# Kernel tuning notes

Hardware: AMD Instinct MI355X
Metric: run time of the kernel (lower is better)

Reference implementation:

```python
import jax, jax.numpy as jnp
import numpy as np

D_MODEL = 768
D_STATE = 16
B, L = 4, 2048


def setup_inputs() -> dict:
    key = jax.random.key(0)
    ks = jax.random.split(key, 8)
    s = 1.0 / np.sqrt(D_MODEL)
    x = jax.random.normal(ks[0], (B, L, D_MODEL), jnp.float32)
    W_in = jax.random.normal(ks[1], (D_MODEL, 2 * D_MODEL), jnp.float32) * s
    b_in = jnp.zeros((2 * D_MODEL,), jnp.float32)
    W_B = jax.random.normal(ks[2], (D_MODEL, D_STATE), jnp.float32) * s
    b_B = jnp.zeros((D_STATE,), jnp.float32)
    W_C = jax.random.normal(ks[3], (D_MODEL, D_STATE), jnp.float32) * s
    b_C = jnp.zeros((D_STATE,), jnp.float32)
    W_delta = jax.random.normal(ks[4], (D_MODEL, D_MODEL), jnp.float32) * s
    b_delta = jnp.zeros((D_MODEL,), jnp.float32)
    W_out = jax.random.normal(ks[5], (D_MODEL, D_MODEL), jnp.float32) * s
    b_out = jnp.zeros((D_MODEL,), jnp.float32)
    # A_log init from the module: log(A + 1) with A[s, d] = s+1
    A_log = jnp.log(jnp.arange(1, D_STATE + 1, dtype=jnp.float32)[:, None]
                    * jnp.ones((1, D_MODEL), jnp.float32) + 1.0)
    D = jnp.ones((D_MODEL,), jnp.float32)
    return {"x": x, "W_in": W_in, "b_in": b_in, "W_B": W_B, "b_B": b_B,
            "W_C": W_C, "b_C": b_C, "W_delta": W_delta, "b_delta": b_delta,
            "W_out": W_out, "b_out": b_out, "A_log": A_log, "D": D}


def reference(x, W_in, b_in, W_B, b_B, W_C, b_C, W_delta, b_delta,
              W_out, b_out, A_log, D):
    x_proj = x @ W_in + b_in                      # (B, L, 2*d_model)
    x_main, x_gate = jnp.split(x_proj, 2, axis=-1)
    x_main = jax.nn.silu(x_main)
    B_mat = x_main @ W_B + b_B                    # (B, L, d_state)
    C_mat = x_main @ W_C + b_C                    # (B, L, d_state)
    delta = jax.nn.softplus(x_main @ W_delta + b_delta) + 0.0001
    delta = jnp.clip(delta, 0.0001, 1.0)          # (B, L, d_model)
    A = jnp.clip(-jnp.exp(A_log), -5.0, -0.1)     # (d_state, d_model)
    deltaA = jnp.exp(jnp.clip(delta[:, :, None, :] * A[None, None, :, :], -2.0, 0.0))
    deltaA = jnp.clip(deltaA, 0.05, 1.0)          # (B, L, d_state, d_model)
    deltaB_u = jnp.clip(delta[:, :, None, :] * B_mat[:, :, :, None] * x_main[:, :, None, :],
                        -5.0, 5.0)                # (B, L, d_state, d_model)

    def binary_operator(elem1, elem2):
        A1, Bu1 = elem1
        A2, Bu2 = elem2
        A_c = jnp.clip(A2 * A1, 1e-06, 10.0)
        Bu_c = jnp.clip(A2 * Bu1 + Bu2, -100.0, 100.0)
        return (A_c, Bu_c)

    # elementwise combine => scanning along axis=1 of the batched arrays is
    # identical to vmapping a per-batch scan over axis 0
    _, h_Bu = jax.lax.associative_scan(binary_operator, (deltaA, deltaB_u), axis=1)
    y = jnp.einsum('blsd,bls->bld', h_Bu, C_mat)
    y = jnp.clip(y, -10.0, 10.0)
    y = y + x_main * D[None, None, :]
    y = y * jax.nn.silu(x_gate)
    y = jnp.clip(y @ W_out + b_out, -10.0, 10.0)
    return y
```

## Files before the change

kernel.cpp:

```cpp
#include <hip/hip_runtime.h>
#include <hip/hip_bf16.h>
#include <cstdint>
#include <cstddef>

#define D_MODEL 768
#define D_STATE 16
#define BB      4
#define LL      2048
#define M_TOT   (BB*LL)
#define NCHUNK  64
#define LCH     (LL/NCHUNK)
#define N_DBC   896

typedef __attribute__((ext_vector_type(8))) short bf16x8;
typedef __attribute__((ext_vector_type(4))) float f32x4;

__device__ __forceinline__ float clampf_(float x, float lo, float hi) {
    return fminf(fmaxf(x, lo), hi);
}
__device__ __forceinline__ float siluf_(float x) {
    return x / (1.f + __expf(-x));
}
__device__ __forceinline__ unsigned short f2bf(float f) {
    unsigned u = __float_as_uint(f);
    u += 0x7fffu + ((u >> 16) & 1u);
    return (unsigned short)(u >> 16);
}
__device__ __forceinline__ float bf2f(unsigned short u) {
    return __uint_as_float(((unsigned)u) << 16);
}
__device__ __forceinline__ void gload16(void* lds, const void* g) {
    __builtin_amdgcn_global_load_lds(
        (const __attribute__((address_space(1))) void*)g,
        (__attribute__((address_space(3))) void*)lds, 16, 0, 0);
}


__global__ __launch_bounds__(256) void k_convert_x(const float* __restrict__ x,
                                                   unsigned short* __restrict__ xb, int n4) {
    int i = blockIdx.x * 256 + threadIdx.x;
    if (i >= n4) return;
    float4 v = ((const float4*)x)[i];
    ushort4 o;
    o.x = f2bf(v.x); o.y = f2bf(v.y); o.z = f2bf(v.z); o.w = f2bf(v.w);
    ((ushort4*)xb)[i] = o;
}

__global__ __launch_bounds__(256) void k_prep_A(const float* __restrict__ A_log,
                                                float* __restrict__ A_cl, int n) {
    int i = blockIdx.x * 256 + threadIdx.x;
    if (i < n) A_cl[i] = clampf_(-__expf(A_log[i]), -5.f, -0.1f);
}

__global__ __launch_bounds__(256) void k_transpose_bf16(const float* __restrict__ src,
                                                        unsigned short* __restrict__ dst,
                                                        int R, int C) {
    __shared__ float tile[32][33];
    int tx = threadIdx.x & 31, ty = threadIdx.x >> 5;
    int c0 = blockIdx.x * 32, r0 = blockIdx.y * 32;
    #pragma unroll
    for (int rr = ty; rr < 32; rr += 8)
        tile[rr][tx] = src[(size_t)(r0 + rr) * C + c0 + tx];
    __syncthreads();
    #pragma unroll
    for (int rr = ty; rr < 32; rr += 8)
        dst[(size_t)(c0 + rr) * R + r0 + tx] = f2bf(tile[tx][rr]);
}

__global__ __launch_bounds__(256) void k_fill_bc(const float* __restrict__ W_B,
                                                 const float* __restrict__ W_C,
                                                 unsigned short* __restrict__ WdBC) {
    int idx = blockIdx.x * 256 + threadIdx.x;
    if (idx >= 128 * D_MODEL) return;
    int r = idx / D_MODEL + D_MODEL, k = idx % D_MODEL;
    unsigned short v = 0;
    if (r < D_MODEL + 16)       v = f2bf(W_B[k * 16 + (r - D_MODEL)]);
    else if (r < D_MODEL + 32)  v = f2bf(W_C[k * 16 + (r - D_MODEL - 16)]);
    WdBC[(size_t)r * D_MODEL + k] = v;
}

__global__ __launch_bounds__(256) void k_bias_dbc(const float* __restrict__ b_delta,
                                                  const float* __restrict__ b_B,
                                                  const float* __restrict__ b_C,
                                                  float* __restrict__ bias) {
    int i = blockIdx.x * 256 + threadIdx.x;
    if (i >= N_DBC) return;
    float v = 0.f;
    if (i < D_MODEL)            v = b_delta[i];
    else if (i < D_MODEL + 16)  v = b_B[i - D_MODEL];
    else if (i < D_MODEL + 32)  v = b_C[i - D_MODEL - 16];
    bias[i] = v;
}

template<int EPI>
__global__ __launch_bounds__(256) void k_gemm(const unsigned short* __restrict__ A,
                                              const unsigned short* __restrict__ Bt,
                                              const float* __restrict__ bias,
                                              int K,
                                              float* __restrict__ out_f,
                                              float* __restrict__ out_f2,
                                              unsigned short* __restrict__ out_b0,
                                              unsigned short* __restrict__ out_b1) {
    __shared__ __align__(16) unsigned short As[128 * 32];
    __shared__ __align__(16) unsigned short Bs[128 * 32];
    const int tid = threadIdx.x;
    const int wave = tid >> 6, lane = tid & 63;
    const int wm = wave >> 1, wn = wave & 1;
    const int m0 = blockIdx.y * 128, n0 = blockIdx.x * 128;
    const int lr = lane & 15, lk = (lane >> 4) * 8;

    f32x4 acc[4][4] = {};

    for (int kt = 0; kt < K; kt += 32) {
        #pragma unroll
        for (int p = 0; p < 2; ++p) {
            int ci = p * 256 + wave * 64 + lane;
            int row = ci >> 2, k8 = (ci & 3) * 8;
            const unsigned short* ga = &A [(size_t)(m0 + row) * K + kt + k8];
            const unsigned short* gb = &Bt[(size_t)(n0 + row) * K + kt + k8];
            gload16(&As[(p * 256 + wave * 64) * 8], ga);
            gload16(&Bs[(p * 256 + wave * 64) * 8], gb);
        }
        __syncthreads();

        bf16x8 af[4], bfr[4];
        #pragma unroll
        for (int mt = 0; mt < 4; ++mt)
            af[mt] = *(const bf16x8*)&As[(wm * 64 + mt * 16 + lr) * 32 + lk];
        #pragma unroll
        for (int nt = 0; nt < 4; ++nt)
            bfr[nt] = *(const bf16x8*)&Bs[(wn * 64 + nt * 16 + lr) * 32 + lk];
        #pragma unroll
        for (int mt = 0; mt < 4; ++mt)
            #pragma unroll
            for (int nt = 0; nt < 4; ++nt)
                acc[mt][nt] = __builtin_amdgcn_mfma_f32_16x16x32_bf16(
                    af[mt], bfr[nt], acc[mt][nt], 0, 0, 0);
        __syncthreads();
    }

    #pragma unroll
    for (int mt = 0; mt < 4; ++mt) {
        int row = m0 + wm * 64 + mt * 16 + (lane >> 4) * 4;
        #pragma unroll
        for (int nt = 0; nt < 4; ++nt) {
            int col = n0 + wn * 64 + nt * 16 + (lane & 15);
            #pragma unroll
            for (int i = 0; i < 4; ++i) {
                int r = row + i;
                float v = acc[mt][nt][i] + bias[col];
                if (EPI == 0) {
                    float s = siluf_(v);
                    if (col < D_MODEL) out_b0[(size_t)r * D_MODEL + col] = f2bf(s);
                    else               out_b1[(size_t)r * D_MODEL + (col - D_MODEL)] = f2bf(s);
                } else if (EPI == 1) {
                    if (col < D_MODEL) {
                        float sp = (v > 20.f) ? v : log1pf(__expf(v));
                        out_b0[(size_t)r * D_MODEL + col] = f2bf(clampf_(sp + 1e-4f, 1e-4f, 1.f));
                    } else if (col < D_MODEL + 16) {
                        out_f[(size_t)r * D_STATE + (col - D_MODEL)] = v;
                    } else if (col < D_MODEL + 32) {
                        out_f2[(size_t)r * D_STATE + (col - D_MODEL - 16)] = v;
                    }
                } else {
                    out_f[(size_t)r * D_MODEL + col] = clampf_(v, -10.f, 10.f);
                }
            }
        }
    }
}

__global__ __launch_bounds__(256) void k_scanA(const unsigned short* __restrict__ dlt,
                                               const unsigned short* __restrict__ xm,
                                               const float* __restrict__ Bm,
                                               const float* __restrict__ A_cl,
                                               float* __restrict__ h_end,
                                               float* __restrict__ Aprod) {
    const int d = blockIdx.x * 256 + threadIdx.x;
    const int c = blockIdx.y, b = blockIdx.z;
    __shared__ float Bsh[LCH][D_STATE];
    const int rowbase = b * LL + c * LCH;
    for (int i = threadIdx.x; i < LCH * D_STATE; i += 256)
        ((float*)Bsh)[i] = Bm[(size_t)rowbase * D_STATE + i];
    __syncthreads();

    float Asv[16], h[16], ap[16];
    #pragma unroll
    for (int s = 0; s < 16; ++s) {
        Asv[s] = A_cl[s * D_MODEL + d];
        h[s] = 0.f; ap[s] = 1.f;
    }
    for (int tt = 0; tt < LCH; ++tt) {
        const size_t rowoff = (size_t)(rowbase + tt);
        float dltv = bf2f(dlt[rowoff * D_MODEL + d]);
        float xv   = bf2f(xm [rowoff * D_MODEL + d]);
        float dx = dltv * xv;
        #pragma unroll
        for (int s = 0; s < 16; ++s) {
            float dA  = __expf(fmaxf(dltv * Asv[s], -2.f));
            float dBu = clampf_(dx * Bsh[tt][s], -5.f, 5.f);
            h[s] = clampf_(fmaf(dA, h[s], dBu), -100.f, 100.f);
            ap[s] *= dA;
        }
    }
    const size_t off = (((size_t)b * NCHUNK + c) * D_STATE) * D_MODEL + d;
    #pragma unroll
    for (int s = 0; s < 16; ++s) {
        h_end[off + (size_t)s * D_MODEL] = h[s];
        Aprod[off + (size_t)s * D_MODEL] = ap[s];
    }
}

__global__ __launch_bounds__(256) void k_scanB(const float* __restrict__ h_end,
                                               const float* __restrict__ Aprod,
                                               float* __restrict__ h_in) {
    const int idx = blockIdx.x * 256 + threadIdx.x;
    const int d = idx % D_MODEL;
    const int rest = idx / D_MODEL;
    const int s = rest & 15, b = rest >> 4;
    float hc = 0.f;
    for (int c = 0; c < NCHUNK; ++c) {
        const size_t off = (((size_t)b * NCHUNK + c) * D_STATE + s) * D_MODEL + d;
        h_in[off] = hc;
        hc = Aprod[off] * hc + h_end[off];
    }
}

__global__ __launch_bounds__(256) void k_scanC(const unsigned short* __restrict__ dlt,
                                               const unsigned short* __restrict__ xm,
                                               const float* __restrict__ Bm,
                                               const float* __restrict__ Cm,
                                               const float* __restrict__ A_cl,
                                               const float* __restrict__ h_in,
                                               const float* __restrict__ Dvec,
                                               const unsigned short* __restrict__ gate,
                                               unsigned short* __restrict__ ymid) {
    const int d = blockIdx.x * 256 + threadIdx.x;
    const int c = blockIdx.y, b = blockIdx.z;
    __shared__ float Bsh[LCH][D_STATE];
    __shared__ float Csh[LCH][D_STATE];
    const int rowbase = b * LL + c * LCH;
    for (int i = threadIdx.x; i < LCH * D_STATE; i += 256) {
        ((float*)Bsh)[i] = Bm[(size_t)rowbase * D_STATE + i];
        ((float*)Csh)[i] = Cm[(size_t)rowbase * D_STATE + i];
    }
    __syncthreads();

    float Asv[16], h[16];
    const size_t coff = (((size_t)b * NCHUNK + c) * D_STATE) * D_MODEL + d;
    #pragma unroll
    for (int s = 0; s < 16; ++s) {
        Asv[s] = A_cl[s * D_MODEL + d];
        h[s] = h_in[coff + (size_t)s * D_MODEL];
    }
    const float Dv = Dvec[d];
    for (int tt = 0; tt < LCH; ++tt) {
        const size_t rowoff = (size_t)(rowbase + tt);
        float dltv = bf2f(dlt[rowoff * D_MODEL + d]);
        float xv   = bf2f(xm [rowoff * D_MODEL + d]);
        float dx = dltv * xv;
        float y = 0.f;
        #pragma unroll
        for (int s = 0; s < 16; ++s) {
            float dA  = __expf(fmaxf(dltv * Asv[s], -2.f));
            float dBu = clampf_(dx * Bsh[tt][s], -5.f, 5.f);
            h[s] = clampf_(fmaf(dA, h[s], dBu), -100.f, 100.f);
            y = fmaf(h[s], Csh[tt][s], y);
        }
        y = clampf_(y, -10.f, 10.f);
        y = fmaf(xv, Dv, y);
        y *= bf2f(gate[rowoff * D_MODEL + d]);
        ymid[rowoff * D_MODEL + d] = f2bf(y);
    }
}

extern "C" void kernel_launch(void* const* d_in, const int* in_sizes, int n_in,
                              void* d_out, int out_size, void* d_ws, size_t ws_size,
                              hipStream_t stream) {
    const float* x       = (const float*)d_in[0];
    const float* W_in    = (const float*)d_in[1];
    const float* b_in    = (const float*)d_in[2];
    const float* W_B     = (const float*)d_in[3];
    const float* b_B     = (const float*)d_in[4];
    const float* W_C     = (const float*)d_in[5];
    const float* b_C     = (const float*)d_in[6];
    const float* W_delta = (const float*)d_in[7];
    const float* b_delta = (const float*)d_in[8];
    const float* W_out   = (const float*)d_in[9];
    const float* b_out   = (const float*)d_in[10];
    const float* A_log   = (const float*)d_in[11];
    const float* Dvec    = (const float*)d_in[12];
    float* out = (float*)d_out;

    char* p = (char*)d_ws;
    auto alloc = [&](size_t bytes) {
        char* r = p;
        p += (bytes + 255) & ~(size_t)255;
        return r;
    };
    unsigned short* xb    = (unsigned short*)alloc((size_t)M_TOT * D_MODEL * 2);
    unsigned short* Wint  = (unsigned short*)alloc((size_t)2 * D_MODEL * D_MODEL * 2);
    unsigned short* WdBC  = (unsigned short*)alloc((size_t)N_DBC * D_MODEL * 2);
    unsigned short* Wot   = (unsigned short*)alloc((size_t)D_MODEL * D_MODEL * 2);
    float*          bdbc  = (float*)alloc((size_t)N_DBC * 4);
    unsigned short* xm_b  = (unsigned short*)alloc((size_t)M_TOT * D_MODEL * 2);
    unsigned short* gate_b= (unsigned short*)alloc((size_t)M_TOT * D_MODEL * 2);
    unsigned short* dlt_b = (unsigned short*)alloc((size_t)M_TOT * D_MODEL * 2);
    float*          Bm    = (float*)alloc((size_t)M_TOT * D_STATE * 4);
    float*          Cm    = (float*)alloc((size_t)M_TOT * D_STATE * 4);
    float*          A_cl  = (float*)alloc((size_t)D_STATE * D_MODEL * 4);
    float*          h_end = (float*)alloc((size_t)BB * NCHUNK * D_STATE * D_MODEL * 4);
    float*          Aprod = (float*)alloc((size_t)BB * NCHUNK * D_STATE * D_MODEL * 4);
    float*          h_in  = (float*)alloc((size_t)BB * NCHUNK * D_STATE * D_MODEL * 4);
    unsigned short* ymid  = (unsigned short*)alloc((size_t)M_TOT * D_MODEL * 2);

    k_convert_x<<<(M_TOT * D_MODEL / 4 + 255) / 256, 256, 0, stream>>>(x, xb, M_TOT * D_MODEL / 4);
    k_prep_A<<<(D_STATE * D_MODEL + 255) / 256, 256, 0, stream>>>(A_log, A_cl, D_STATE * D_MODEL);
    k_transpose_bf16<<<dim3(2 * D_MODEL / 32, D_MODEL / 32), 256, 0, stream>>>(W_in, Wint, D_MODEL, 2 * D_MODEL);
    k_transpose_bf16<<<dim3(D_MODEL / 32, D_MODEL / 32), 256, 0, stream>>>(W_delta, WdBC, D_MODEL, D_MODEL);
    k_fill_bc<<<(128 * D_MODEL + 255) / 256, 256, 0, stream>>>(W_B, W_C, WdBC);
    k_bias_dbc<<<(N_DBC + 255) / 256, 256, 0, stream>>>(b_delta, b_B, b_C, bdbc);
    k_transpose_bf16<<<dim3(D_MODEL / 32, D_MODEL / 32), 256, 0, stream>>>(W_out, Wot, D_MODEL, D_MODEL);

    k_gemm<0><<<dim3(2 * D_MODEL / 128, M_TOT / 128), 256, 0, stream>>>(
        xb, Wint, b_in, D_MODEL, nullptr, nullptr, xm_b, gate_b);
    k_gemm<1><<<dim3(N_DBC / 128, M_TOT / 128), 256, 0, stream>>>(
        xm_b, WdBC, bdbc, D_MODEL, Bm, Cm, dlt_b, nullptr);
    k_scanA<<<dim3(D_MODEL / 256, NCHUNK, BB), 256, 0, stream>>>(dlt_b, xm_b, Bm, A_cl, h_end, Aprod);
    k_scanB<<<(BB * D_STATE * D_MODEL) / 256, 256, 0, stream>>>(h_end, Aprod, h_in);
    k_scanC<<<dim3(D_MODEL / 256, NCHUNK, BB), 256, 0, stream>>>(
        dlt_b, xm_b, Bm, Cm, A_cl, h_in, Dvec, gate_b, ymid);
    k_gemm<2><<<dim3(D_MODEL / 128, M_TOT / 128), 256, 0, stream>>>(
        ymid, Wot, b_out, D_MODEL, out, nullptr, nullptr, nullptr);
}
```

Baseline: 224.1 us.

## Double-buffer GEMM LDS tiles and swizzle workgroup order across XCDs

```diff
diff --git a/kernel.cpp b/kernel.cpp
--- a/kernel.cpp
+++ b/kernel.cpp
@@ -96,48 +96,67 @@
 __global__ __launch_bounds__(256) void k_gemm(const unsigned short* __restrict__ A,
                                               const unsigned short* __restrict__ Bt,
                                               const float* __restrict__ bias,
-                                              int K,
+                                              int K, int gx,
                                               float* __restrict__ out_f,
                                               float* __restrict__ out_f2,
                                               unsigned short* __restrict__ out_b0,
                                               unsigned short* __restrict__ out_b1) {
-    __shared__ __align__(16) unsigned short As[128 * 32];
-    __shared__ __align__(16) unsigned short Bs[128 * 32];
+    __shared__ __align__(16) unsigned short As[2][128 * 32];
+    __shared__ __align__(16) unsigned short Bs[2][128 * 32];
     const int tid = threadIdx.x;
     const int wave = tid >> 6, lane = tid & 63;
     const int wm = wave >> 1, wn = wave & 1;
-    const int m0 = blockIdx.y * 128, n0 = blockIdx.x * 128;
+
+    const int nwg = gridDim.x;
+    const int wg = blockIdx.x;
+    int swz = wg;
+    if ((nwg & 7) == 0) {
+        const int q = nwg >> 3;
+        swz = (wg & 7) * q + (wg >> 3);
+    }
+    const int bx = swz % gx, by = swz / gx;
+    const int m0 = by * 128, n0 = bx * 128;
     const int lr = lane & 15, lk = (lane >> 4) * 8;
 
     f32x4 acc[4][4] = {};
 
-    for (int kt = 0; kt < K; kt += 32) {
+    auto stage = [&](int buf, int kt) {
         #pragma unroll
         for (int p = 0; p < 2; ++p) {
             int ci = p * 256 + wave * 64 + lane;
             int row = ci >> 2, k8 = (ci & 3) * 8;
-            const unsigned short* ga = &A [(size_t)(m0 + row) * K + kt + k8];
-            const unsigned short* gb = &Bt[(size_t)(n0 + row) * K + kt + k8];
-            gload16(&As[(p * 256 + wave * 64) * 8], ga);
-            gload16(&Bs[(p * 256 + wave * 64) * 8], gb);
+            gload16(&As[buf][(p * 256 + wave * 64) * 8],
+                    &A [(size_t)(m0 + row) * K + kt + k8]);
+            gload16(&Bs[buf][(p * 256 + wave * 64) * 8],
+                    &Bt[(size_t)(n0 + row) * K + kt + k8]);
         }
-        __syncthreads();
-
+    };
+    auto compute = [&](int buf) {
         bf16x8 af[4], bfr[4];
         #pragma unroll
         for (int mt = 0; mt < 4; ++mt)
-            af[mt] = *(const bf16x8*)&As[(wm * 64 + mt * 16 + lr) * 32 + lk];
+            af[mt] = *(const bf16x8*)&As[buf][(wm * 64 + mt * 16 + lr) * 32 + lk];
         #pragma unroll
         for (int nt = 0; nt < 4; ++nt)
-            bfr[nt] = *(const bf16x8*)&Bs[(wn * 64 + nt * 16 + lr) * 32 + lk];
+            bfr[nt] = *(const bf16x8*)&Bs[buf][(wn * 64 + nt * 16 + lr) * 32 + lk];
         #pragma unroll
         for (int mt = 0; mt < 4; ++mt)
             #pragma unroll
             for (int nt = 0; nt < 4; ++nt)
                 acc[mt][nt] = __builtin_amdgcn_mfma_f32_16x16x32_bf16(
                     af[mt], bfr[nt], acc[mt][nt], 0, 0, 0);
+    };
+
+    stage(0, 0);
+    __syncthreads();
+    int cur = 0;
+    for (int kt = 32; kt < K; kt += 32) {
+        stage(cur ^ 1, kt);
+        compute(cur);
         __syncthreads();
-    }
+        cur ^= 1;
+    }
+    compute(cur);
 
     #pragma unroll
     for (int mt = 0; mt < 4; ++mt) {
@@ -322,14 +341,14 @@
     k_bias_dbc<<<(N_DBC + 255) / 256, 256, 0, stream>>>(b_delta, b_B, b_C, bdbc);
     k_transpose_bf16<<<dim3(D_MODEL / 32, D_MODEL / 32), 256, 0, stream>>>(W_out, Wot, D_MODEL, D_MODEL);
 
-    k_gemm<0><<<dim3(2 * D_MODEL / 128, M_TOT / 128), 256, 0, stream>>>(
-        xb, Wint, b_in, D_MODEL, nullptr, nullptr, xm_b, gate_b);
-    k_gemm<1><<<dim3(N_DBC / 128, M_TOT / 128), 256, 0, stream>>>(
-        xm_b, WdBC, bdbc, D_MODEL, Bm, Cm, dlt_b, nullptr);
+    k_gemm<0><<<dim3((2 * D_MODEL / 128) * (M_TOT / 128)), 256, 0, stream>>>(
+        xb, Wint, b_in, D_MODEL, 2 * D_MODEL / 128, nullptr, nullptr, xm_b, gate_b);
+    k_gemm<1><<<dim3((N_DBC / 128) * (M_TOT / 128)), 256, 0, stream>>>(
+        xm_b, WdBC, bdbc, D_MODEL, N_DBC / 128, Bm, Cm, dlt_b, nullptr);
     k_scanA<<<dim3(D_MODEL / 256, NCHUNK, BB), 256, 0, stream>>>(dlt_b, xm_b, Bm, A_cl, h_end, Aprod);
     k_scanB<<<(BB * D_STATE * D_MODEL) / 256, 256, 0, stream>>>(h_end, Aprod, h_in);
     k_scanC<<<dim3(D_MODEL / 256, NCHUNK, BB), 256, 0, stream>>>(
         dlt_b, xm_b, Bm, Cm, A_cl, h_in, Dvec, gate_b, ymid);
-    k_gemm<2><<<dim3(D_MODEL / 128, M_TOT / 128), 256, 0, stream>>>(
-        ymid, Wot, b_out, D_MODEL, out, nullptr, nullptr, nullptr);
-}
+    k_gemm<2><<<dim3((D_MODEL / 128) * (M_TOT / 128)), 256, 0, stream>>>(
+        ymid, Wot, b_out, D_MODEL, D_MODEL / 128, out, nullptr, nullptr, nullptr);
+}
```

Measured after the change: 214.9 us. 4.1% less time.
